# Kernel optimization log

Hardware: AMD Instinct MI355X
Metric: run time of the kernel (lower is better)

Reference implementation:

```python
import jax, jax.numpy as jnp
import numpy as np

N = 40          # grid side
DT = 1.0        # time step
LEAKY = 0.03    # leaky rate


def setup_inputs() -> dict:
    key = jax.random.key(0)
    k1, = jax.random.split(key, 1)
    n = N
    c0, dc, crr, CN = 300.0, -250.0 / n, 0.8, 0.1
    # replicate the torch init: column-dependent wave speed with random relative perturbation
    c = c0 * jnp.ones((n, n), jnp.float32) + dc * (jnp.arange(n, dtype=jnp.float32) - 1.0)[None, :]
    c = c - crr * jax.random.uniform(k1, (n, n), jnp.float32) * c
    dx = (DT / CN) * jnp.max(c) * np.float32(np.sqrt(2.0)) * jnp.ones((n, n), jnp.float32)
    return {
        "c": c,
        "k": jnp.zeros((n, n), jnp.float32),
        "kp": 1e-4 * jnp.ones((n, n), jnp.float32),
        "dx": dx,
        "dy": dx,
    }


def reference(c, k, kp, dx, dy):
    n = N
    g = n * n                      # grid_size
    s = 3 * g                      # state_size
    sp = jax.nn.softplus
    c_pos = sp(c).reshape(-1)      # [g]
    k_x = sp(k).reshape(-1)        # [g] (k_y identical in original)
    kp_p = sp(kp).reshape(-1)      # [g]
    # dx, dy are passed but unused by the eigendecomposition (faithful to source)

    xi = jnp.float32(np.pi / 2.0)  # xi_magnitude = pi / (2*1.0)
    lam1 = 1.0 / (1.0 + DT * k_x)                                   # [g] real
    real_part = 0.5 * (1.0 / (1.0 + DT * kp_p) + lam1)
    imag_part = c_pos * DT * xi / jnp.sqrt((1.0 + DT * kp_p) * (1.0 + DT * k_x))
    lam2 = (real_part + 1j * imag_part).astype(jnp.complex64)
    lam3 = jnp.conj(lam2)
    Lambda = jnp.concatenate([lam1.astype(jnp.complex64), lam2, lam3])  # [3g]

    beta = DT / (1.0 + DT * k_x)
    alpha = lam2 - lam1.astype(jnp.complex64) + 1e-6
    v2 = (beta.astype(jnp.complex64) * 1j * xi) / alpha   # v2_2 == v2_3
    v3 = -jnp.conj(v2)                                    # v3_2 == v3_3

    ones_c = jnp.ones(g, jnp.complex64)
    Z = jnp.zeros((g, g), jnp.complex64)
    D = jnp.diag
    # block-diagonal-structured eigenvector matrix, [3g, 3g]
    P = jnp.block([
        [D(ones_c), D(ones_c), D(ones_c)],
        [Z,         D(v2),     D(v3)],
        [Z,         D(v2),     D(v3)],
    ])
    # A = Re(P @ diag(Lambda) @ P^H); P @ diag(L) is column scaling
    A = ((P * Lambda[None, :]) @ jnp.conj(P).T).real
    W = (A - (1.0 - LEAKY) * jnp.eye(s, dtype=A.dtype)) / LEAKY
    return (A, W, c_pos.reshape(n, n), k)
```

## Files before the change

kernel.cpp:

```cpp
#include <hip/hip_runtime.h>
#include <math.h>


constexpr int       GN = 40;
constexpr int       G  = GN * GN;
constexpr int       S  = 3 * G;
constexpr long long SS = (long long)S * S;
constexpr int       ROW4 = S / 4;

__device__ __forceinline__ float softplus_f(float x) {
    return fmaxf(x, 0.0f) + log1pf(expf(-fabsf(x)));
}

__global__ __launch_bounds__(256) void eigen_rows_kernel(
        const float* __restrict__ c,
        const float* __restrict__ k,
        const float* __restrict__ kp,
        float* __restrict__ out) {
    int r = blockIdx.x;

    if (r >= 2 * S) {
        for (int i = threadIdx.x; i < G; i += 256) {
            out[2 * SS + i]     = softplus_f(c[i]);
            out[2 * SS + G + i] = k[i];
        }
        return;
    }

    bool isW = r >= S;
    int  rr  = isW ? r - S : r;
    int  b   = rr / G;
    int  g   = rr % G;

    float c_pos = softplus_f(c[g]);
    float k_x   = softplus_f(k[g]);
    float kp_p  = softplus_f(kp[g]);

    const float xi = 1.57079632679489662f;
    float okx  = 1.0f + k_x;
    float okp  = 1.0f + kp_p;
    float lam1 = 1.0f / okx;
    float rp   = 0.5f * (1.0f / okp + lam1);
    float im   = c_pos * xi / sqrtf(okp * okx);
    float ar   = rp - lam1 + 1e-6f;
    float bx   = lam1 * xi;
    float v2sq = bx * bx / (ar * ar + im * im);

    float d1 = lam1 + 2.0f * rp;
    float d2 = 2.0f * v2sq * rp;

    const float INV_L = 1.0f / 0.03f;
    const float OML   = 0.97f;

    int   c1, c2;
    float v1, v2v;
    if (b == 0) {
        c1 = g;      v1 = isW ? (d1 - OML) * INV_L : d1;
        c2 = -1;     v2v = 0.0f;
    } else if (b == 1) {
        c1 = G + g;      v1  = isW ? (d2 - OML) * INV_L : d2;
        c2 = 2 * G + g;  v2v = isW ? d2 * INV_L : d2;
    } else {
        c1 = G + g;      v1  = isW ? d2 * INV_L : d2;
        c2 = 2 * G + g;  v2v = isW ? (d2 - OML) * INV_L : d2;
    }

    float4* __restrict__ row4 = (float4*)out + (long long)r * ROW4;
    for (int i4 = threadIdx.x; i4 < ROW4; i4 += 256) {
        int c0 = i4 * 4;
        float4 v;
        v.x = (c0     == c1) ? v1 : ((c0     == c2) ? v2v : 0.0f);
        v.y = (c0 + 1 == c1) ? v1 : ((c0 + 1 == c2) ? v2v : 0.0f);
        v.z = (c0 + 2 == c1) ? v1 : ((c0 + 2 == c2) ? v2v : 0.0f);
        v.w = (c0 + 3 == c1) ? v1 : ((c0 + 3 == c2) ? v2v : 0.0f);
        row4[i4] = v;
    }
}

extern "C" void kernel_launch(void* const* d_in, const int* in_sizes, int n_in,
                              void* d_out, int out_size, void* d_ws, size_t ws_size,
                              hipStream_t stream) {
    const float* c  = (const float*)d_in[0];
    const float* k  = (const float*)d_in[1];
    const float* kp = (const float*)d_in[2];
    float* out = (float*)d_out;

    eigen_rows_kernel<<<2 * S + 1, 256, 0, stream>>>(c, k, kp, out);
}
```

Baseline: 32.73 us.

## Flatten output into grid-stride float4 loop with fixed block count

```diff
diff --git a/kernel.cpp b/kernel.cpp
--- a/kernel.cpp
+++ b/kernel.cpp
@@ -2,78 +2,99 @@
 #include <math.h>
 
 
-constexpr int       GN = 40;
-constexpr int       G  = GN * GN;
-constexpr int       S  = 3 * G;
-constexpr long long SS = (long long)S * S;
-constexpr int       ROW4 = S / 4;
+constexpr int       GN   = 40;
+constexpr int       G    = GN * GN;
+constexpr int       S    = 3 * G;
+constexpr long long SS   = (long long)S * S;
+constexpr unsigned  ROW4 = S / 4;
+constexpr unsigned  SS4  = (unsigned)(SS / 4);
+constexpr unsigned  TOT4 = 2 * SS4 + (2 * G) / 4;
 
 __device__ __forceinline__ float softplus_f(float x) {
     return fmaxf(x, 0.0f) + log1pf(expf(-fabsf(x)));
 }
 
-__global__ __launch_bounds__(256) void eigen_rows_kernel(
+__global__ __launch_bounds__(256) void eigen_flat_kernel(
         const float* __restrict__ c,
         const float* __restrict__ k,
         const float* __restrict__ kp,
         float* __restrict__ out) {
-    int r = blockIdx.x;
+    unsigned i      = blockIdx.x * 256u + threadIdx.x;
+    unsigned stride = gridDim.x * 256u;
+    float4* __restrict__ out4 = (float4*)out;
 
-    if (r >= 2 * S) {
-        for (int i = threadIdx.x; i < G; i += 256) {
-            out[2 * SS + i]     = softplus_f(c[i]);
-            out[2 * SS + G + i] = k[i];
+    for (; i < TOT4; i += stride) {
+        if (i >= 2 * SS4) {
+            unsigned base = (i - 2 * SS4) * 4;
+            float4 v;
+            float* vv = &v.x;
+#pragma unroll
+            for (int j = 0; j < 4; ++j) {
+                unsigned idx = base + j;
+                vv[j] = (idx < (unsigned)G) ? softplus_f(c[idx]) : k[idx - G];
+            }
+            out4[i] = v;
+            continue;
         }
-        return;
-    }
 
-    bool isW = r >= S;
-    int  rr  = isW ? r - S : r;
-    int  b   = rr / G;
-    int  g   = rr % G;
+        bool     isW = i >= SS4;
+        unsigned fr  = isW ? i - SS4 : i;
+        unsigned r   = fr / ROW4;
+        unsigned i4  = fr - r * ROW4;
+        unsigned b   = r / (unsigned)G;
+        unsigned g   = r - b * (unsigned)G;
 
-    float c_pos = softplus_f(c[g]);
-    float k_x   = softplus_f(k[g]);
-    float kp_p  = softplus_f(kp[g]);
+        unsigned q1, q2;
+        if (b == 0) { q1 = g >> 2;                   q2 = 0xffffffffu; }
+        else        { q1 = ((unsigned)G + g) >> 2;   q2 = (2u * G + g) >> 2; }
 
-    const float xi = 1.57079632679489662f;
-    float okx  = 1.0f + k_x;
-    float okp  = 1.0f + kp_p;
-    float lam1 = 1.0f / okx;
-    float rp   = 0.5f * (1.0f / okp + lam1);
-    float im   = c_pos * xi / sqrtf(okp * okx);
-    float ar   = rp - lam1 + 1e-6f;
-    float bx   = lam1 * xi;
-    float v2sq = bx * bx / (ar * ar + im * im);
+        float4 v = make_float4(0.f, 0.f, 0.f, 0.f);
 
-    float d1 = lam1 + 2.0f * rp;
-    float d2 = 2.0f * v2sq * rp;
+        if (i4 == q1 || i4 == q2) {
+            float c_pos = softplus_f(c[g]);
+            float k_x   = softplus_f(k[g]);
+            float kp_p  = softplus_f(kp[g]);
 
-    const float INV_L = 1.0f / 0.03f;
-    const float OML   = 0.97f;
+            const float xi = 1.57079632679489662f;
+            float okx  = 1.0f + k_x;
+            float okp  = 1.0f + kp_p;
+            float lam1 = 1.0f / okx;
+            float rp   = 0.5f * (1.0f / okp + lam1);
+            float im   = c_pos * xi / sqrtf(okp * okx);
+            float ar   = rp - lam1 + 1e-6f;
+            float bx   = lam1 * xi;
+            float v2sq = bx * bx / (ar * ar + im * im);
 
-    int   c1, c2;
-    float v1, v2v;
-    if (b == 0) {
-        c1 = g;      v1 = isW ? (d1 - OML) * INV_L : d1;
-        c2 = -1;     v2v = 0.0f;
-    } else if (b == 1) {
-        c1 = G + g;      v1  = isW ? (d2 - OML) * INV_L : d2;
-        c2 = 2 * G + g;  v2v = isW ? d2 * INV_L : d2;
-    } else {
-        c1 = G + g;      v1  = isW ? d2 * INV_L : d2;
-        c2 = 2 * G + g;  v2v = isW ? (d2 - OML) * INV_L : d2;
-    }
+            float d1 = lam1 + 2.0f * rp;
+            float d2 = 2.0f * v2sq * rp;
 
-    float4* __restrict__ row4 = (float4*)out + (long long)r * ROW4;
-    for (int i4 = threadIdx.x; i4 < ROW4; i4 += 256) {
-        int c0 = i4 * 4;
-        float4 v;
-        v.x = (c0     == c1) ? v1 : ((c0     == c2) ? v2v : 0.0f);
-        v.y = (c0 + 1 == c1) ? v1 : ((c0 + 1 == c2) ? v2v : 0.0f);
-        v.z = (c0 + 2 == c1) ? v1 : ((c0 + 2 == c2) ? v2v : 0.0f);
-        v.w = (c0 + 3 == c1) ? v1 : ((c0 + 3 == c2) ? v2v : 0.0f);
-        row4[i4] = v;
+            const float INV_L = 1.0f / 0.03f;
+            const float OML   = 0.97f;
+
+            unsigned c1, c2;
+            float    v1, v2v;
+            if (b == 0) {
+                c1 = g;                 v1  = isW ? (d1 - OML) * INV_L : d1;
+                c2 = 0xffffffffu;       v2v = 0.0f;
+            } else if (b == 1) {
+                c1 = (unsigned)G + g;   v1  = isW ? (d2 - OML) * INV_L : d2;
+                c2 = 2u * G + g;        v2v = isW ? d2 * INV_L : d2;
+            } else {
+                c1 = (unsigned)G + g;   v1  = isW ? d2 * INV_L : d2;
+                c2 = 2u * G + g;        v2v = isW ? (d2 - OML) * INV_L : d2;
+            }
+
+            unsigned c0 = i4 * 4;
+            float* vv = &v.x;
+#pragma unroll
+            for (int j = 0; j < 4; ++j) {
+                unsigned col = c0 + j;
+                if (col == c1)      vv[j] = v1;
+                else if (col == c2) vv[j] = v2v;
+            }
+        }
+
+        out4[i] = v;
     }
 }
 
@@ -85,5 +106,5 @@
     const float* kp = (const float*)d_in[2];
     float* out = (float*)d_out;
 
-    eigen_rows_kernel<<<2 * S + 1, 256, 0, stream>>>(c, k, kp, out);
+    eigen_flat_kernel<<<2048, 256, 0, stream>>>(c, k, kp, out);
 }
```

After: 32.99 us. About the same (+0.8%).

## Replace per-row blocks with flat chunked zero-fill plus sparse nonzero patch

Applied to the files above, without the earlier changes.

```diff
diff --git a/kernel.cpp b/kernel.cpp
--- a/kernel.cpp
+++ b/kernel.cpp
@@ -2,78 +2,104 @@
 #include <math.h>
 
 
-constexpr int       GN = 40;
-constexpr int       G  = GN * GN;
-constexpr int       S  = 3 * G;
-constexpr long long SS = (long long)S * S;
-constexpr int       ROW4 = S / 4;
+constexpr int       GN    = 40;
+constexpr int       G     = GN * GN;
+constexpr int       S     = 3 * G;
+constexpr long long SS    = (long long)S * S;
+constexpr unsigned  ROW4  = S / 4;
+constexpr unsigned  SS4   = (unsigned)(SS / 4);
+constexpr unsigned  REGION = 2 * SS4;
+constexpr unsigned  TOT4  = REGION + (2 * G) / 4;
+constexpr unsigned  NB    = 2048;
+constexpr unsigned  IT    = 22;
+constexpr unsigned  CHUNK = IT * 256;
 
 __device__ __forceinline__ float softplus_f(float x) {
     return fmaxf(x, 0.0f) + log1pf(expf(-fabsf(x)));
 }
 
-__global__ __launch_bounds__(256) void eigen_rows_kernel(
+__global__ __launch_bounds__(256) void eigen_chunk_kernel(
         const float* __restrict__ c,
         const float* __restrict__ k,
         const float* __restrict__ kp,
         float* __restrict__ out) {
-    int r = blockIdx.x;
+    const unsigned bid = blockIdx.x, tid = threadIdx.x;
+    const unsigned lo  = bid * CHUNK;
+    float4* __restrict__ out4 = (float4*)out;
+    const float4 z = make_float4(0.f, 0.f, 0.f, 0.f);
 
-    if (r >= 2 * S) {
-        for (int i = threadIdx.x; i < G; i += 256) {
-            out[2 * SS + i]     = softplus_f(c[i]);
-            out[2 * SS + G + i] = k[i];
-        }
-        return;
+    if (lo + CHUNK <= REGION) {
+        float4* p = out4 + lo + tid;
+#pragma unroll
+        for (unsigned it = 0; it < IT; ++it) p[it * 256u] = z;
+    } else {
+        for (unsigned idx = lo + tid; idx < REGION; idx += 256u) out4[idx] = z;
     }
 
-    bool isW = r >= S;
-    int  rr  = isW ? r - S : r;
-    int  b   = rr / G;
-    int  g   = rr % G;
-
-    float c_pos = softplus_f(c[g]);
-    float k_x   = softplus_f(k[g]);
-    float kp_p  = softplus_f(kp[g]);
-
-    const float xi = 1.57079632679489662f;
-    float okx  = 1.0f + k_x;
-    float okp  = 1.0f + kp_p;
-    float lam1 = 1.0f / okx;
-    float rp   = 0.5f * (1.0f / okp + lam1);
-    float im   = c_pos * xi / sqrtf(okp * okx);
-    float ar   = rp - lam1 + 1e-6f;
-    float bx   = lam1 * xi;
-    float v2sq = bx * bx / (ar * ar + im * im);
-
-    float d1 = lam1 + 2.0f * rp;
-    float d2 = 2.0f * v2sq * rp;
-
-    const float INV_L = 1.0f / 0.03f;
-    const float OML   = 0.97f;
-
-    int   c1, c2;
-    float v1, v2v;
-    if (b == 0) {
-        c1 = g;      v1 = isW ? (d1 - OML) * INV_L : d1;
-        c2 = -1;     v2v = 0.0f;
-    } else if (b == 1) {
-        c1 = G + g;      v1  = isW ? (d2 - OML) * INV_L : d2;
-        c2 = 2 * G + g;  v2v = isW ? d2 * INV_L : d2;
-    } else {
-        c1 = G + g;      v1  = isW ? d2 * INV_L : d2;
-        c2 = 2 * G + g;  v2v = isW ? (d2 - OML) * INV_L : d2;
+    if (bid == NB - 1) {
+        for (unsigned t = tid; t < 2u * G; t += 256u)
+            out[2 * SS + t] = (t < (unsigned)G) ? softplus_f(c[t]) : k[t - G];
     }
 
-    float4* __restrict__ row4 = (float4*)out + (long long)r * ROW4;
-    for (int i4 = threadIdx.x; i4 < ROW4; i4 += 256) {
-        int c0 = i4 * 4;
-        float4 v;
-        v.x = (c0     == c1) ? v1 : ((c0     == c2) ? v2v : 0.0f);
-        v.y = (c0 + 1 == c1) ? v1 : ((c0 + 1 == c2) ? v2v : 0.0f);
-        v.z = (c0 + 2 == c1) ? v1 : ((c0 + 2 == c2) ? v2v : 0.0f);
-        v.w = (c0 + 3 == c1) ? v1 : ((c0 + 3 == c2) ? v2v : 0.0f);
-        row4[i4] = v;
+    __syncthreads();
+
+    if (lo >= REGION) return;
+    const unsigned hi = (lo + CHUNK < REGION) ? lo + CHUNK : REGION;
+
+    if (tid < 24) {
+        unsigned region = tid / 12;
+        unsigned slot   = (tid % 12) / 2;
+        unsigned spec   = tid & 1;
+        unsigned off    = region * SS4;
+
+        unsigned ilo = lo > off ? lo : off;
+        unsigned ihi = hi < off + SS4 ? hi : off + SS4;
+        if (ilo < ihi) {
+            unsigned r    = (ilo - off) / ROW4 + slot;
+            unsigned rmax = (ihi - 1 - off) / ROW4;
+            if (r <= rmax && r < (unsigned)S) {
+                unsigned b = r / (unsigned)G;
+                unsigned g = r - b * (unsigned)G;
+                bool valid = (b != 0) || (spec == 0);
+                if (valid) {
+                    unsigned col = (b == 0) ? g
+                                 : (spec == 0 ? (unsigned)G + g : 2u * G + g);
+                    unsigned p_abs = off + r * ROW4 + (col >> 2);
+                    if (p_abs >= lo && p_abs < hi) {
+                        float c_pos = softplus_f(c[g]);
+                        float k_x   = softplus_f(k[g]);
+                        float kp_p  = softplus_f(kp[g]);
+
+                        const float xi = 1.57079632679489662f;
+                        float okx  = 1.0f + k_x;
+                        float okp  = 1.0f + kp_p;
+                        float lam1 = 1.0f / okx;
+                        float rp   = 0.5f * (1.0f / okp + lam1);
+                        float im   = c_pos * xi / sqrtf(okp * okx);
+                        float ar   = rp - lam1 + 1e-6f;
+                        float bx   = lam1 * xi;
+                        float v2sq = bx * bx / (ar * ar + im * im);
+
+                        float d1 = lam1 + 2.0f * rp;
+                        float d2 = 2.0f * v2sq * rp;
+
+                        const float INV_L = 1.0f / 0.03f;
+                        const float OML   = 0.97f;
+
+                        float base = (b == 0) ? d1 : d2;
+                        bool  diag = (b == 0) || (b == 1 && spec == 0)
+                                               || (b == 2 && spec == 1);
+                        float val  = region ? (diag ? (base - OML) * INV_L
+                                                    : base * INV_L)
+                                            : base;
+
+                        float4 v = z;
+                        (&v.x)[col & 3] = val;
+                        out4[p_abs] = v;
+                    }
+                }
+            }
+        }
     }
 }
 
@@ -85,5 +111,5 @@
     const float* kp = (const float*)d_in[2];
     float* out = (float*)d_out;
 
-    eigen_rows_kernel<<<2 * S + 1, 256, 0, stream>>>(c, k, kp, out);
+    eigen_chunk_kernel<<<NB, 256, 0, stream>>>(c, k, kp, out);
 }
```

Result: slower. 37.02 us (+13.1%).
